# Performance work log

Measured on AMD Instinct MI355X. Metric: run time of the kernel, lower is better.

The kernel has to match this reference:

```python
import jax, jax.numpy as jnp
import numpy as np
from jax import lax

B, S, FEAT, OUT = 64, 8192, 8, 64


def setup_inputs() -> dict:
    key = jax.random.key(0)
    ks = jax.random.split(key, 7)
    x = jax.random.normal(ks[0], (B, S, FEAT), dtype=jnp.float32)
    # torch default init: U(-1/sqrt(fan_in), 1/sqrt(fan_in))
    def uinit(k, shape, fan_in):
        bound = 1.0 / np.sqrt(fan_in)
        return jax.random.uniform(k, shape, jnp.float32, -bound, bound)
    W1 = uinit(ks[1], (32, 1, 2, 2), 1 * 2 * 2)   # OIHW
    b1 = uinit(ks[2], (32,), 1 * 2 * 2)
    W2 = uinit(ks[3], (32, 32, 1, 2), 32 * 1 * 2)
    b2 = uinit(ks[4], (32,), 32 * 1 * 2)
    Wp = uinit(ks[5], (OUT, 64), 64)              # torch Linear: [out, in]
    bp = uinit(ks[6], (OUT,), 64)
    return {"x": x, "W1": W1, "b1": b1, "W2": W2, "b2": b2, "Wp": Wp, "bp": bp}


def reference(x, W1, b1, W2, b2, Wp, bp):
    b, s, _ = x.shape
    xg = x.reshape(b * s, 1, 2, 4)  # [N,1,2,4] NCHW
    dn = ("NCHW", "OIHW", "NCHW")
    h = lax.conv_general_dilated(xg, W1, (1, 1), "VALID", dimension_numbers=dn)
    h = jax.nn.relu(h + b1[None, :, None, None])          # [N,32,1,3]
    h = lax.conv_general_dilated(h, W2, (1, 1), "VALID", dimension_numbers=dn)
    h = jax.nn.relu(h + b2[None, :, None, None])          # [N,32,1,2]
    h = h.reshape(b * s, 64)                              # C*H*W flatten, matches torch
    out = h @ Wp.T + bp                                   # [N,64]
    return out.reshape(b, s, -1)
```

## Files before the change

kernel.cpp:

```cpp
#include <hip/hip_runtime.h>

typedef __attribute__((ext_vector_type(8))) __bf16 bf16x8;
typedef __attribute__((ext_vector_type(8))) ushort ushort8;
typedef __attribute__((ext_vector_type(4))) float floatx4;

union FragU { ushort8 u; bf16x8 b; };

__device__ inline ushort bf1(float a){
  unsigned u = __float_as_uint(a);
  return (ushort)((u + 0x7FFFu + ((u >> 16) & 1u)) >> 16);
}
__device__ inline unsigned bfpack(float lo, float hi){
  return (unsigned)bf1(lo) | ((unsigned)bf1(hi) << 16);
}

#define BLOCKS 1024

__global__ __launch_bounds__(256) void cnn_fused(
    const float* __restrict__ x,  const float* __restrict__ W1,
    const float* __restrict__ b1, const float* __restrict__ W2,
    const float* __restrict__ b2, const float* __restrict__ Wp,
    const float* __restrict__ bp, float* __restrict__ out, int niter)
{
  __shared__ __align__(16) ushort h2buf[4 * 16 * 72];
  const int tid  = threadIdx.x;
  const int wid  = tid >> 6;
  const int lane = tid & 63;
  const int lm   = lane & 15;
  const int quad = lane >> 4;
  ushort*   myh2 = &h2buf[wid * (16 * 72)];
  unsigned* h2d  = (unsigned*)myh2;

  FragU w2f[2][2];
  #pragma unroll
  for (int t = 0; t < 2; ++t)
    #pragma unroll
    for (int h = 0; h < 2; ++h)
      #pragma unroll
      for (int j = 0; j < 8; ++j)
        w2f[t][h].u[j] = bf1(W2[(t*16 + lm)*64 + (quad*8 + j)*2 + h]);

  FragU wpf[4][2];
  #pragma unroll
  for (int t = 0; t < 4; ++t)
    #pragma unroll
    for (int h = 0; h < 2; ++h)
      #pragma unroll
      for (int j = 0; j < 8; ++j){
        const int c   = h*32 + quad*8 + j;
        const int cp  = c & 31;
        const int oc2 = (cp >> 1) | ((cp & 1) << 4);
        wpf[t][h].u[j] = bf1(Wp[(4*lm + t)*64 + oc2*2 + h]);
      }

  float w1r[8][4], b1r[8];
  #pragma unroll
  for (int i = 0; i < 8; ++i){
    const int oc = quad*8 + i;
    w1r[i][0] = W1[oc*4+0]; w1r[i][1] = W1[oc*4+1];
    w1r[i][2] = W1[oc*4+2]; w1r[i][3] = W1[oc*4+3];
    b1r[i]    = b1[oc];
  }
  const float  b2a = b2[lm], b2b = b2[16 + lm];
  const float4 bp4 = ((const float4*)bp)[lm];

  const long gw   = (long)blockIdx.x * 4 + wid;
  long tilebase   = gw * ((long)niter * 16);

  const float4* x4 = (const float4*)x;
  float4 xa = x4[2*(tilebase + lm)];
  float4 xb = x4[2*(tilebase + lm) + 1];

  const floatx4 z = {0.f, 0.f, 0.f, 0.f};

  for (int it = 0; it < niter; ++it){
    float4 nxa, nxb;
    if (it + 1 < niter){
      const long nr = tilebase + 16 + lm;
      nxa = x4[2*nr]; nxb = x4[2*nr + 1];
    }

    FragU F0, F1, F2;
    #pragma unroll
    for (int i = 0; i < 8; ++i){
      const float w00 = w1r[i][0], w01 = w1r[i][1];
      const float w10 = w1r[i][2], w11 = w1r[i][3], bb = b1r[i];
      F0.u[i] = bf1(fmaxf(0.f, bb + w00*xa.x + w01*xa.y + w10*xb.x + w11*xb.y));
      F1.u[i] = bf1(fmaxf(0.f, bb + w00*xa.y + w01*xa.z + w10*xb.y + w11*xb.z));
      F2.u[i] = bf1(fmaxf(0.f, bb + w00*xa.z + w01*xa.w + w10*xb.z + w11*xb.w));
    }

    floatx4 a00 = z, a01 = z, a10 = z, a11 = z;
    a00 = __builtin_amdgcn_mfma_f32_16x16x32_bf16(F0.b, w2f[0][0].b, a00, 0,0,0);
    a00 = __builtin_amdgcn_mfma_f32_16x16x32_bf16(F1.b, w2f[0][1].b, a00, 0,0,0);
    a01 = __builtin_amdgcn_mfma_f32_16x16x32_bf16(F0.b, w2f[1][0].b, a01, 0,0,0);
    a01 = __builtin_amdgcn_mfma_f32_16x16x32_bf16(F1.b, w2f[1][1].b, a01, 0,0,0);
    a10 = __builtin_amdgcn_mfma_f32_16x16x32_bf16(F1.b, w2f[0][0].b, a10, 0,0,0);
    a10 = __builtin_amdgcn_mfma_f32_16x16x32_bf16(F2.b, w2f[0][1].b, a10, 0,0,0);
    a11 = __builtin_amdgcn_mfma_f32_16x16x32_bf16(F1.b, w2f[1][0].b, a11, 0,0,0);
    a11 = __builtin_amdgcn_mfma_f32_16x16x32_bf16(F2.b, w2f[1][1].b, a11, 0,0,0);

    #pragma unroll
    for (int rg = 0; rg < 4; ++rg){
      const int rr = (quad*4 + rg) * 36;
      h2d[rr +      lm] = bfpack(fmaxf(0.f, a00[rg] + b2a), fmaxf(0.f, a01[rg] + b2b));
      h2d[rr + 16 + lm] = bfpack(fmaxf(0.f, a10[rg] + b2a), fmaxf(0.f, a11[rg] + b2b));
    }
    __syncthreads();

    FragU ca0, ca1;
    ca0.u = *(const ushort8*)&myh2[lm*72 +      quad*8];
    ca1.u = *(const ushort8*)&myh2[lm*72 + 32 + quad*8];

    floatx4 oacc[4];
    #pragma unroll
    for (int t = 0; t < 4; ++t){
      floatx4 acc = z;
      acc = __builtin_amdgcn_mfma_f32_16x16x32_bf16(ca0.b, wpf[t][0].b, acc, 0,0,0);
      acc = __builtin_amdgcn_mfma_f32_16x16x32_bf16(ca1.b, wpf[t][1].b, acc, 0,0,0);
      oacc[t] = acc;
    }

    #pragma unroll
    for (int rg = 0; rg < 4; ++rg){
      float4 v;
      v.x = oacc[0][rg] + bp4.x;
      v.y = oacc[1][rg] + bp4.y;
      v.z = oacc[2][rg] + bp4.z;
      v.w = oacc[3][rg] + bp4.w;
      *(float4*)(out + (tilebase + quad*4 + rg)*64 + 4*lm) = v;
    }
    __syncthreads();

    if (it + 1 < niter){ xa = nxa; xb = nxb; tilebase += 16; }
  }
}

extern "C" void kernel_launch(void* const* d_in, const int* in_sizes, int n_in,
                              void* d_out, int out_size, void* d_ws, size_t ws_size,
                              hipStream_t stream)
{
  const float* x  = (const float*)d_in[0];
  const float* W1 = (const float*)d_in[1];
  const float* b1 = (const float*)d_in[2];
  const float* W2 = (const float*)d_in[3];
  const float* b2 = (const float*)d_in[4];
  const float* Wp = (const float*)d_in[5];
  const float* bp = (const float*)d_in[6];
  float* out = (float*)d_out;

  const int rows  = in_sizes[0] / 8;
  const int tiles = rows / 16;
  const int niter = tiles / (BLOCKS * 4);
  cnn_fused<<<BLOCKS, 256, 0, stream>>>(x, W1, b1, W2, b2, Wp, bp, out, niter);
}
```

Measured before the change: 180.3 us.

## Drop block barriers, use packed bf16 conversion and nontemporal output stores

Removes both __syncthreads per iteration, because each wave uses only its own shared-memory slice, so block-wide barriers are not needed. Replaces the manual bf16 rounding with the packed float2-to-bfloat162 conversion intrinsic, which can map to a single packed convert instruction. Writes outputs with nontemporal stores to reduce cache pollution from the large streaming output. Dropping the barriers relies on implicit ordering within a wave for the LDS write-then-read, which is a correctness risk if the compiler reorders the accesses.

```diff
diff --git a/kernel.cpp b/kernel.cpp
--- a/kernel.cpp
+++ b/kernel.cpp
@@ -1,17 +1,20 @@
 #include <hip/hip_runtime.h>
+#include <hip/hip_bf16.h>
 
 typedef __attribute__((ext_vector_type(8))) __bf16 bf16x8;
 typedef __attribute__((ext_vector_type(8))) ushort ushort8;
 typedef __attribute__((ext_vector_type(4))) float floatx4;
 
-union FragU { ushort8 u; bf16x8 b; };
+union FragU { ushort8 u; bf16x8 b; unsigned d[4]; };
 
 __device__ inline ushort bf1(float a){
   unsigned u = __float_as_uint(a);
   return (ushort)((u + 0x7FFFu + ((u >> 16) & 1u)) >> 16);
 }
-__device__ inline unsigned bfpack(float lo, float hi){
-  return (unsigned)bf1(lo) | ((unsigned)bf1(hi) << 16);
+__device__ inline unsigned cvt_pk(float a, float b){
+  union { __hip_bfloat162 h; unsigned u; } c;
+  c.h = __float22bfloat162_rn(float2{a, b});
+  return c.u;
 }
 
 #define BLOCKS 1024
@@ -64,8 +67,8 @@
   const float  b2a = b2[lm], b2b = b2[16 + lm];
   const float4 bp4 = ((const float4*)bp)[lm];
 
-  const long gw   = (long)blockIdx.x * 4 + wid;
-  long tilebase   = gw * ((long)niter * 16);
+  const long gw = (long)blockIdx.x * 4 + wid;
+  long tilebase = gw * ((long)niter * 16);
 
   const float4* x4 = (const float4*)x;
   float4 xa = x4[2*(tilebase + lm)];
@@ -82,12 +85,20 @@
 
     FragU F0, F1, F2;
     #pragma unroll
-    for (int i = 0; i < 8; ++i){
-      const float w00 = w1r[i][0], w01 = w1r[i][1];
-      const float w10 = w1r[i][2], w11 = w1r[i][3], bb = b1r[i];
-      F0.u[i] = bf1(fmaxf(0.f, bb + w00*xa.x + w01*xa.y + w10*xb.x + w11*xb.y));
-      F1.u[i] = bf1(fmaxf(0.f, bb + w00*xa.y + w01*xa.z + w10*xb.y + w11*xb.z));
-      F2.u[i] = bf1(fmaxf(0.f, bb + w00*xa.z + w01*xa.w + w10*xb.z + w11*xb.w));
+    for (int i = 0; i < 8; i += 2){
+      const float p00 = w1r[i][0],   p01 = w1r[i][1];
+      const float p10 = w1r[i][2],   p11 = w1r[i][3],   pb = b1r[i];
+      const float q00 = w1r[i+1][0], q01 = w1r[i+1][1];
+      const float q10 = w1r[i+1][2], q11 = w1r[i+1][3], qb = b1r[i+1];
+      const float a0 = fmaxf(0.f, pb + p00*xa.x + p01*xa.y + p10*xb.x + p11*xb.y);
+      const float a1 = fmaxf(0.f, pb + p00*xa.y + p01*xa.z + p10*xb.y + p11*xb.z);
+      const float a2 = fmaxf(0.f, pb + p00*xa.z + p01*xa.w + p10*xb.z + p11*xb.w);
+      const float c0 = fmaxf(0.f, qb + q00*xa.x + q01*xa.y + q10*xb.x + q11*xb.y);
+      const float c1 = fmaxf(0.f, qb + q00*xa.y + q01*xa.z + q10*xb.y + q11*xb.z);
+      const float c2 = fmaxf(0.f, qb + q00*xa.z + q01*xa.w + q10*xb.z + q11*xb.w);
+      F0.d[i>>1] = cvt_pk(a0, c0);
+      F1.d[i>>1] = cvt_pk(a1, c1);
+      F2.d[i>>1] = cvt_pk(a2, c2);
     }
 
     floatx4 a00 = z, a01 = z, a10 = z, a11 = z;
@@ -103,10 +114,9 @@
     #pragma unroll
     for (int rg = 0; rg < 4; ++rg){
       const int rr = (quad*4 + rg) * 36;
-      h2d[rr +      lm] = bfpack(fmaxf(0.f, a00[rg] + b2a), fmaxf(0.f, a01[rg] + b2b));
-      h2d[rr + 16 + lm] = bfpack(fmaxf(0.f, a10[rg] + b2a), fmaxf(0.f, a11[rg] + b2b));
+      h2d[rr +      lm] = cvt_pk(fmaxf(0.f, a00[rg] + b2a), fmaxf(0.f, a01[rg] + b2b));
+      h2d[rr + 16 + lm] = cvt_pk(fmaxf(0.f, a10[rg] + b2a), fmaxf(0.f, a11[rg] + b2b));
     }
-    __syncthreads();
 
     FragU ca0, ca1;
     ca0.u = *(const ushort8*)&myh2[lm*72 +      quad*8];
@@ -123,14 +133,13 @@
 
     #pragma unroll
     for (int rg = 0; rg < 4; ++rg){
-      float4 v;
-      v.x = oacc[0][rg] + bp4.x;
-      v.y = oacc[1][rg] + bp4.y;
-      v.z = oacc[2][rg] + bp4.z;
-      v.w = oacc[3][rg] + bp4.w;
-      *(float4*)(out + (tilebase + quad*4 + rg)*64 + 4*lm) = v;
+      floatx4 v;
+      v[0] = oacc[0][rg] + bp4.x;
+      v[1] = oacc[1][rg] + bp4.y;
+      v[2] = oacc[2][rg] + bp4.z;
+      v[3] = oacc[3][rg] + bp4.w;
+      __builtin_nontemporal_store(v, (floatx4*)(out + (tilebase + quad*4 + rg)*64 + 4*lm));
     }
-    __syncthreads();
 
     if (it + 1 < niter){ xa = nxa; xb = nxb; tilebase += 16; }
   }
```

Result: no change. 181.5 us (+0.7%).
